# Kernel tuning notes

Hardware: AMD Instinct MI355X
Metric: run time of the kernel (lower is better)

Reference implementation:

```python
import jax, jax.numpy as jnp
import numpy as np

N, E = 10000, 320000
MUL0, MUL1 = 64, 32  # 64x0e + 32x1o
SQ3 = 3.0 ** 0.5
SQ2 = 2.0 ** 0.5


def ssp(v):  # shifted softplus
    return jax.nn.softplus(v) - jnp.log(2.0)


def mlp2(v, W1, W2):  # e3nn FullyConnectedNet style: /sqrt(fan_in), no bias, act between
    h = ssp(v @ (W1 / jnp.sqrt(1.0 * W1.shape[0])))
    return h @ (W2 / jnp.sqrt(1.0 * W2.shape[0]))


def linear_rs(x0, x1, W0, b0, W1):  # per-irrep-type linear with 1/sqrt(fan_in) rescale
    y0 = x0 @ (W0 / jnp.sqrt(1.0 * W0.shape[0])) + b0
    y1 = jnp.einsum('nui,uv->nvi', x1, W1) / jnp.sqrt(1.0 * W1.shape[0])
    return y0, y1


def forward(x, edge_sh, edge_attr, W0p, b0p, W1p, W0n, b0n, W1n, G1, g1b, G2, g2b, F1, F2, L1, L2, WO0, bO0, WO1, WO2, edge_index):
    dst, src = edge_index[0], edge_index[1]
    x0 = x[:, :MUL0]                      # [N,64] scalars
    x1 = x[:, MUL0:].reshape(N, MUL1, 3)  # [N,32,3] l=1 vectors
    # linear_node_pre, then invariant edge features s0 (scalars of dst/src + l1 inner products)
    p0, p1 = linear_rs(x0, x1, W0p, b0p, W1p)
    ip1 = jnp.sum(p1[dst] * p1[src], -1) / SQ3          # [E,32]
    s0 = jnp.concatenate([p0[dst], p0[src], ip1], -1)   # [E,160]
    # NormGate: gate scalars + l1 norms through a 2-layer SiLU MLP
    n1 = jnp.sqrt(jnp.sum(x1 * x1, -1) + 1e-12)         # [N,32]
    f0 = jnp.concatenate([x0, n1], -1)                  # [N,96]
    g = jax.nn.silu(f0 @ G1 + g1b) @ G2 + g2b           # [N,96]
    x0g, x1g = g[:, :MUL0], x1 * g[:, MUL0:, None]
    # linear_node
    x0n, x1n = linear_rs(x0g, x1g, W0n, b0n, W1n)
    # per-edge tensor-product weights: fc_node(edge_attr) * layer_l0(s0)
    w = mlp2(edge_attr, F1, F2) * mlp2(s0, L1, L2)      # [E,224]
    w1, w2, w3, w4, w5 = w[:, :64], w[:, 64:128], w[:, 128:160], w[:, 160:192], w[:, 192:224]
    xs0, xs1 = x0n[src], x1n[src]                       # gather source nodes
    sh0, sh1 = edge_sh[:, 0], edge_sh[:, 1:4]
    # depthwise 'uvu' tensor product paths (w3j constants for l<=1)
    o0a = w1 * xs0 * sh0[:, None]                                        # (0e,0e)->0e  [E,64]
    o0b = w4 * jnp.sum(xs1 * sh1[:, None, :], -1) / SQ3                  # (1o,1o)->0e  [E,32]
    o1a = w2[:, :, None] * xs0[:, :, None] * sh1[:, None, :] / SQ3       # (0e,1o)->1o  [E,64,3]
    o1b = w3[:, :, None] * xs1 * sh0[:, None, None]                      # (1o,0e)->1o  [E,32,3]
    o1c = w5[:, :, None] * jnp.cross(xs1, jnp.broadcast_to(sh1[:, None, :], xs1.shape)) / SQ2  # (1o,1o)->1e [E,32,3]
    ef = jnp.concatenate([o0a, o0b, o1a.reshape(E, -1), o1b.reshape(E, -1), o1c.reshape(E, -1)], -1)  # [E,480]
    out = jax.ops.segment_sum(ef, dst, num_segments=N)  # scatter-add over dst
    # linear_out: 96x0e + 96x1o + 32x1e -> 128x0e + 64x1o + 32x1e
    t0 = out[:, :96]
    t1 = out[:, 96:384].reshape(N, 96, 3)
    t2 = out[:, 384:].reshape(N, 32, 3)
    y0 = t0 @ (WO0 / jnp.sqrt(96.0)) + bO0
    y1 = jnp.einsum('nui,uv->nvi', t1, WO1) / jnp.sqrt(96.0)
    y2 = jnp.einsum('nui,uv->nvi', t2, WO2) / jnp.sqrt(32.0)
    return jnp.concatenate([y0, y1.reshape(N, -1), y2.reshape(N, -1)], -1)  # [N,416]


def setup_inputs():
    key = jax.random.key(0)
    ks = jax.random.split(key, 20)
    rn = lambda k, s: jax.random.normal(k, s, dtype=jnp.float32)
    z = lambda n: jnp.zeros((n,), jnp.float32)
    return dict(
        x=rn(ks[0], (N, 160)),
        edge_sh=rn(ks[1], (E, 4)),
        edge_attr=rn(ks[2], (E, 32)),
        W0p=rn(ks[3], (64, 64)), b0p=z(64), W1p=rn(ks[4], (32, 32)),
        W0n=rn(ks[5], (64, 64)), b0n=z(64), W1n=rn(ks[6], (32, 32)),
        G1=rn(ks[7], (96, 96)) / 96 ** 0.5, g1b=z(96),
        G2=rn(ks[8], (96, 96)) / 96 ** 0.5, g2b=z(96),
        F1=rn(ks[9], (32, 32)), F2=rn(ks[10], (32, 224)),
        L1=rn(ks[11], (160, 32)), L2=rn(ks[12], (32, 224)),
        WO0=rn(ks[13], (96, 128)), bO0=z(128),
        WO1=rn(ks[14], (96, 64)), WO2=rn(ks[15], (32, 32)),
        edge_index=jax.random.randint(ks[16], (2, E), 0, N),
    )


def reference(x, edge_sh, edge_attr, W0p, b0p, W1p, W0n, b0n, W1n, G1, g1b, G2, g2b, F1, F2, L1, L2, WO0, bO0, WO1, WO2, edge_index):
    return forward(x, edge_sh, edge_attr, W0p, b0p, W1p, W0n, b0n, W1n, G1, g1b, G2, g2b, F1, F2, L1, L2, WO0, bO0, WO1, WO2, edge_index)
```

## Files before the change

kernel.cpp:

```cpp
#include <hip/hip_runtime.h>
#include <math.h>

#define NN 10000
#define EE 320000
#define TILE 32

constexpr float INVS32  = 0.17677669529663687f;
constexpr float INVS160 = 0.07905694150420949f;
constexpr float INVS96  = 0.10206207261596575f;
constexpr float INVS3   = 0.5773502691896258f;
constexpr float INVS2   = 0.7071067811865476f;
constexpr float LN2     = 0.6931471805599453f;

typedef short bf16x8 __attribute__((ext_vector_type(8)));
typedef float f32x4  __attribute__((ext_vector_type(4)));

__device__ __forceinline__ float sspf(float v) {
  return fmaxf(v, 0.f) + __logf(1.f + __expf(-fabsf(v))) - LN2;
}
__device__ __forceinline__ ushort f2bf(float f) {
  union { float f; unsigned u; } v; v.f = f;
  unsigned r = v.u + 0x7FFF + ((v.u >> 16) & 1);
  return (ushort)(r >> 16);
}
__device__ __forceinline__ float bf2f(ushort u) {
  return __uint_as_float(((unsigned)u) << 16);
}
__device__ __forceinline__ unsigned pk(float a, float b) {
  return (unsigned)f2bf(a) | ((unsigned)f2bf(b) << 16);
}

__global__ __launch_bounds__(1024) void scan_k(const int* __restrict__ cnt,
                                               int* __restrict__ cursor) {
  __shared__ int s[1024];
  const int t = threadIdx.x;
  int loc[10];
  int sum = 0;
#pragma unroll
  for (int jj = 0; jj < 10; ++jj) {
    int idx = t * 10 + jj;
    int c = (idx < NN) ? cnt[idx] : 0;
    loc[jj] = sum;
    sum += c;
  }
  s[t] = sum;
  __syncthreads();
  for (int d = 1; d < 1024; d <<= 1) {
    int v = (t >= d) ? s[t - d] : 0;
    __syncthreads();
    s[t] += v;
    __syncthreads();
  }
  const int excl = (t > 0) ? s[t - 1] : 0;
#pragma unroll
  for (int jj = 0; jj < 10; ++jj) {
    int idx = t * 10 + jj;
    if (idx < NN) cursor[idx] = excl + loc[jj];
  }
}

__global__ void prep_t_k(const float* __restrict__ F2, const float* __restrict__ L2,
                         const float* __restrict__ WO0, const float* __restrict__ WO1,
                         const float* __restrict__ WO2,
                         const float* __restrict__ F1, const float* __restrict__ L1,
                         const int* __restrict__ ei, int* __restrict__ cnt,
                         ushort* __restrict__ F2Tb, ushort* __restrict__ L2Tb,
                         float* __restrict__ WO0T, float* __restrict__ WO1T,
                         float* __restrict__ WO2T,
                         ushort* __restrict__ F1Tb, ushort* __restrict__ L1cTb) {
  int i = blockIdx.x * 256 + threadIdx.x;
  if (i < EE) atomicAdd(&cnt[ei[i]], 1);
  if (i < 7168) {
    int c = i >> 5, k = i & 31;
    float sc = (c < 64)  ? (1.f / 32.f)
             : (c < 128) ? (INVS3 / 32.f)
             : (c < 160) ? (1.f / 32.f)
             : (c < 192) ? (INVS3 / 32.f)
                         : (INVS2 / 32.f);
    F2Tb[i] = f2bf(F2[k * 224 + c] * sc);
    L2Tb[i] = f2bf(L2[k * 224 + c]);
  } else if (i < 7168 + 12288) {
    int j = i - 7168; int k = j / 96, u = j - k * 96;
    WO0T[j] = WO0[u * 128 + k] * INVS96;
  } else if (i < 7168 + 12288 + 6144) {
    int j = i - 7168 - 12288; int v = j / 96, u = j - v * 96;
    WO1T[j] = WO1[u * 64 + v] * INVS96;
  } else if (i < 7168 + 12288 + 6144 + 1024) {
    int j = i - 7168 - 12288 - 6144; int v = j >> 5, u = j & 31;
    WO2T[j] = WO2[u * 32 + v] * INVS32;
  } else if (i < 26624 + 1024) {
    int j = i - 26624; int n = j >> 5, k = j & 31;
    F1Tb[j] = f2bf(F1[k * 32 + n] * INVS32);
  } else if (i < 27648 + 1024) {
    int j = i - 27648; int n = j >> 5, k = j & 31;
    L1cTb[j] = f2bf(L1[(128 + k) * 32 + n] * INVS160);
  }
}

__global__ __launch_bounds__(64) void node_prep_k(
    const float* __restrict__ x,
    const float* __restrict__ W0p, const float* __restrict__ b0p,
    const float* __restrict__ W1p,
    const float* __restrict__ W0n, const float* __restrict__ b0n,
    const float* __restrict__ W1n,
    const float* __restrict__ G1, const float* __restrict__ g1b,
    const float* __restrict__ G2, const float* __restrict__ g2b,
    const float* __restrict__ L1,
    const int* __restrict__ ei, int* __restrict__ cursor, int* __restrict__ order,
    float* __restrict__ p1w, ushort* __restrict__ x0nb, ushort* __restrict__ x1nb,
    float* __restrict__ Aw, float* __restrict__ Bw)
{
  {
    int gid = blockIdx.x * 64 + threadIdx.x;
#pragma unroll
    for (int r = 0; r < 2; ++r) {
      int e = gid + r * 160000;
      int p = atomicAdd(&cursor[ei[e]], 1);
      order[p] = e;
    }
  }

  const int lane = threadIdx.x;
  const int nb = blockIdx.x * 4;

  __shared__ float sX[4][160];
  __shared__ float sP0[4][64];
  __shared__ float sF0[4][96];
  __shared__ float sH1[4][96];
  __shared__ float sG[4][96];

#pragma unroll
  for (int j = 0; j < 4; ++j) {
    const int n = nb + j;
    sX[j][lane]      = x[n * 160 + lane];
    sX[j][lane + 64] = x[n * 160 + lane + 64];
    if (lane < 32) sX[j][lane + 128] = x[n * 160 + lane + 128];
  }

  {
    float a0 = 0.f, a1 = 0.f, a2 = 0.f, a3 = 0.f;
    for (int i = 0; i < 64; ++i) {
      const float w = W0p[i * 64 + lane];
      a0 = fmaf(sX[0][i], w, a0); a1 = fmaf(sX[1][i], w, a1);
      a2 = fmaf(sX[2][i], w, a2); a3 = fmaf(sX[3][i], w, a3);
    }
    const float b = b0p[lane];
    sP0[0][lane] = a0 * 0.125f + b; sP0[1][lane] = a1 * 0.125f + b;
    sP0[2][lane] = a2 * 0.125f + b; sP0[3][lane] = a3 * 0.125f + b;
#pragma unroll
    for (int j = 0; j < 4; ++j) sF0[j][lane] = sX[j][lane];
  }

  {
    const int o = lane; const int v = o / 3, i_ = o - 3 * v;
    float a0 = 0.f, a1 = 0.f, a2 = 0.f, a3 = 0.f;
    for (int u = 0; u < 32; ++u) {
      const float w = W1p[u * 32 + v];
      a0 = fmaf(sX[0][64 + u * 3 + i_], w, a0);
      a1 = fmaf(sX[1][64 + u * 3 + i_], w, a1);
      a2 = fmaf(sX[2][64 + u * 3 + i_], w, a2);
      a3 = fmaf(sX[3][64 + u * 3 + i_], w, a3);
    }
    p1w[(size_t)(nb + 0) * 96 + o] = a0 * INVS32;
    p1w[(size_t)(nb + 1) * 96 + o] = a1 * INVS32;
    p1w[(size_t)(nb + 2) * 96 + o] = a2 * INVS32;
    p1w[(size_t)(nb + 3) * 96 + o] = a3 * INVS32;
  }
  if (lane < 32) {
    const int o = 64 + lane; const int v = o / 3, i_ = o - 3 * v;
    float a0 = 0.f, a1 = 0.f, a2 = 0.f, a3 = 0.f;
    for (int u = 0; u < 32; ++u) {
      const float w = W1p[u * 32 + v];
      a0 = fmaf(sX[0][64 + u * 3 + i_], w, a0);
      a1 = fmaf(sX[1][64 + u * 3 + i_], w, a1);
      a2 = fmaf(sX[2][64 + u * 3 + i_], w, a2);
      a3 = fmaf(sX[3][64 + u * 3 + i_], w, a3);
    }
    p1w[(size_t)(nb + 0) * 96 + o] = a0 * INVS32;
    p1w[(size_t)(nb + 1) * 96 + o] = a1 * INVS32;
    p1w[(size_t)(nb + 2) * 96 + o] = a2 * INVS32;
    p1w[(size_t)(nb + 3) * 96 + o] = a3 * INVS32;
  }

  if (lane < 32) {
#pragma unroll
    for (int j = 0; j < 4; ++j) {
      float s2 = 1e-12f;
#pragma unroll
      for (int i = 0; i < 3; ++i) { float t = sX[j][64 + lane * 3 + i]; s2 += t * t; }
      sF0[j][64 + lane] = sqrtf(s2);
    }
  }

  {
    const float b = g1b[lane];
    float a0 = b, a1 = b, a2 = b, a3 = b;
    for (int i = 0; i < 96; ++i) {
      const float w = G1[i * 96 + lane];
      a0 = fmaf(sF0[0][i], w, a0); a1 = fmaf(sF0[1][i], w, a1);
      a2 = fmaf(sF0[2][i], w, a2); a3 = fmaf(sF0[3][i], w, a3);
    }
    sH1[0][lane] = a0 / (1.f + __expf(-a0));
    sH1[1][lane] = a1 / (1.f + __expf(-a1));
    sH1[2][lane] = a2 / (1.f + __expf(-a2));
    sH1[3][lane] = a3 / (1.f + __expf(-a3));
  }
  if (lane < 32) {
    const int o = 64 + lane;
    const float b = g1b[o];
    float a0 = b, a1 = b, a2 = b, a3 = b;
    for (int i = 0; i < 96; ++i) {
      const float w = G1[i * 96 + o];
      a0 = fmaf(sF0[0][i], w, a0); a1 = fmaf(sF0[1][i], w, a1);
      a2 = fmaf(sF0[2][i], w, a2); a3 = fmaf(sF0[3][i], w, a3);
    }
    sH1[0][o] = a0 / (1.f + __expf(-a0));
    sH1[1][o] = a1 / (1.f + __expf(-a1));
    sH1[2][o] = a2 / (1.f + __expf(-a2));
    sH1[3][o] = a3 / (1.f + __expf(-a3));
  }

  {
    const float b = g2b[lane];
    float a0 = b, a1 = b, a2 = b, a3 = b;
    for (int i = 0; i < 96; ++i) {
      const float w = G2[i * 96 + lane];
      a0 = fmaf(sH1[0][i], w, a0); a1 = fmaf(sH1[1][i], w, a1);
      a2 = fmaf(sH1[2][i], w, a2); a3 = fmaf(sH1[3][i], w, a3);
    }
    sG[0][lane] = a0; sG[1][lane] = a1; sG[2][lane] = a2; sG[3][lane] = a3;
  }
  if (lane < 32) {
    const int o = 64 + lane;
    const float b = g2b[o];
    float a0 = b, a1 = b, a2 = b, a3 = b;
    for (int i = 0; i < 96; ++i) {
      const float w = G2[i * 96 + o];
      a0 = fmaf(sH1[0][i], w, a0); a1 = fmaf(sH1[1][i], w, a1);
      a2 = fmaf(sH1[2][i], w, a2); a3 = fmaf(sH1[3][i], w, a3);
    }
    sG[0][o] = a0; sG[1][o] = a1; sG[2][o] = a2; sG[3][o] = a3;
  }

  {
    float a0 = 0.f, a1 = 0.f, a2 = 0.f, a3 = 0.f;
    for (int i = 0; i < 64; ++i) {
      const float w = W0n[i * 64 + lane];
      a0 = fmaf(sG[0][i], w, a0); a1 = fmaf(sG[1][i], w, a1);
      a2 = fmaf(sG[2][i], w, a2); a3 = fmaf(sG[3][i], w, a3);
    }
    const float b = b0n[lane];
    x0nb[(size_t)(nb + 0) * 64 + lane] = f2bf(a0 * 0.125f + b);
    x0nb[(size_t)(nb + 1) * 64 + lane] = f2bf(a1 * 0.125f + b);
    x0nb[(size_t)(nb + 2) * 64 + lane] = f2bf(a2 * 0.125f + b);
    x0nb[(size_t)(nb + 3) * 64 + lane] = f2bf(a3 * 0.125f + b);
  }

  {
    const int o = lane; const int v = o / 3, i_ = o - 3 * v;
    float a0 = 0.f, a1 = 0.f, a2 = 0.f, a3 = 0.f;
    for (int u = 0; u < 32; ++u) {
      const float w = W1n[u * 32 + v];
      a0 = fmaf(sX[0][64 + u * 3 + i_] * sG[0][64 + u], w, a0);
      a1 = fmaf(sX[1][64 + u * 3 + i_] * sG[1][64 + u], w, a1);
      a2 = fmaf(sX[2][64 + u * 3 + i_] * sG[2][64 + u], w, a2);
      a3 = fmaf(sX[3][64 + u * 3 + i_] * sG[3][64 + u], w, a3);
    }
    x1nb[(size_t)(nb + 0) * 96 + o] = f2bf(a0 * INVS32);
    x1nb[(size_t)(nb + 1) * 96 + o] = f2bf(a1 * INVS32);
    x1nb[(size_t)(nb + 2) * 96 + o] = f2bf(a2 * INVS32);
    x1nb[(size_t)(nb + 3) * 96 + o] = f2bf(a3 * INVS32);
  }
  if (lane < 32) {
    const int o = 64 + lane; const int v = o / 3, i_ = o - 3 * v;
    float a0 = 0.f, a1 = 0.f, a2 = 0.f, a3 = 0.f;
    for (int u = 0; u < 32; ++u) {
      const float w = W1n[u * 32 + v];
      a0 = fmaf(sX[0][64 + u * 3 + i_] * sG[0][64 + u], w, a0);
      a1 = fmaf(sX[1][64 + u * 3 + i_] * sG[1][64 + u], w, a1);
      a2 = fmaf(sX[2][64 + u * 3 + i_] * sG[2][64 + u], w, a2);
      a3 = fmaf(sX[3][64 + u * 3 + i_] * sG[3][64 + u], w, a3);
    }
    x1nb[(size_t)(nb + 0) * 96 + o] = f2bf(a0 * INVS32);
    x1nb[(size_t)(nb + 1) * 96 + o] = f2bf(a1 * INVS32);
    x1nb[(size_t)(nb + 2) * 96 + o] = f2bf(a2 * INVS32);
    x1nb[(size_t)(nb + 3) * 96 + o] = f2bf(a3 * INVS32);
  }

  if (lane < 32) {
    float a0 = 0.f, a1 = 0.f, a2 = 0.f, a3 = 0.f;
    float c0 = 0.f, c1 = 0.f, c2 = 0.f, c3 = 0.f;
    for (int i = 0; i < 64; ++i) {
      const float wa = L1[i * 32 + lane];
      const float wb = L1[(64 + i) * 32 + lane];
      a0 = fmaf(sP0[0][i], wa, a0); a1 = fmaf(sP0[1][i], wa, a1);
      a2 = fmaf(sP0[2][i], wa, a2); a3 = fmaf(sP0[3][i], wa, a3);
      c0 = fmaf(sP0[0][i], wb, c0); c1 = fmaf(sP0[1][i], wb, c1);
      c2 = fmaf(sP0[2][i], wb, c2); c3 = fmaf(sP0[3][i], wb, c3);
    }
    Aw[(size_t)(nb + 0) * 32 + lane] = a0 * INVS160;
    Aw[(size_t)(nb + 1) * 32 + lane] = a1 * INVS160;
    Aw[(size_t)(nb + 2) * 32 + lane] = a2 * INVS160;
    Aw[(size_t)(nb + 3) * 32 + lane] = a3 * INVS160;
    Bw[(size_t)(nb + 0) * 32 + lane] = c0 * INVS160;
    Bw[(size_t)(nb + 1) * 32 + lane] = c1 * INVS160;
    Bw[(size_t)(nb + 2) * 32 + lane] = c2 * INVS160;
    Bw[(size_t)(nb + 3) * 32 + lane] = c3 * INVS160;
  }
}

__global__ __launch_bounds__(256, 4) void fused_edge_k(
    const float* __restrict__ edge_attr,
    const float* __restrict__ edge_sh,
    const int* __restrict__ ei,
    const ushort* __restrict__ F1Tb, const ushort* __restrict__ L1cTb,
    const ushort* __restrict__ F2Tb, const ushort* __restrict__ L2Tb,
    const float* __restrict__ p1w, const float* __restrict__ Aw,
    const float* __restrict__ Bw,
    const ushort* __restrict__ x0nb, const ushort* __restrict__ x1nb,
    const int* __restrict__ order,
    float* __restrict__ o480p)
{
  const int s0  = blockIdx.x * TILE;
  const int tid = threadIdx.x;

  __shared__ __align__(16) char uMem[32 * 224 * 2];
  ushort (*sW)[224] = (ushort (*)[224])uMem;
  ushort* sEAb = (ushort*)uMem;
  ushort* sIPb = (ushort*)(uMem + 2560);
  float*  sAB  = (float*)(uMem + 5120);

  __shared__ ushort sHF[32][40];
  __shared__ ushort sHL[32][40];
  __shared__ ushort sXS0[32][64];
  __shared__ ushort sXS1[32][96];
  __shared__ __align__(16) float sSH[32][4];
  __shared__ int    sDst[32];

  const int g = tid >> 3, l = tid & 7;
  const int e   = order[s0 + g];
  const int dst = ei[e];
  const int src = ei[EE + e];
  if (l == 0) sDst[g] = dst;

  {
    float4 ea = *(const float4*)(edge_attr + (size_t)e * 32 + l * 4);
    *(unsigned*)&sEAb[g * 40 + l * 4 + 0] = pk(ea.x, ea.y);
    *(unsigned*)&sEAb[g * 40 + l * 4 + 2] = pk(ea.z, ea.w);
  }
  if (l == 1) *(float4*)&sSH[g][0] = *(const float4*)(edge_sh + (size_t)e * 4);
  {
    uint4 v = *(const uint4*)(x0nb + (size_t)src * 64 + l * 8);
    *(uint4*)&sXS0[g][l * 8] = v;
    const uint2* b2 = (const uint2*)(x1nb + (size_t)src * 96 + l * 12);
    uint2 w0 = b2[0], w1 = b2[1], w2 = b2[2];
    *(uint2*)&sXS1[g][l * 12 + 0] = w0;
    *(uint2*)&sXS1[g][l * 12 + 4] = w1;
    *(uint2*)&sXS1[g][l * 12 + 8] = w2;
  }
  {
    const float4* pd = (const float4*)(p1w + (size_t)dst * 96 + l * 12);
    const float4* ps = (const float4*)(p1w + (size_t)src * 96 + l * 12);
    float dp[12], sp[12];
#pragma unroll
    for (int k = 0; k < 3; ++k) {
      float4 v = pd[k]; dp[4*k] = v.x; dp[4*k+1] = v.y; dp[4*k+2] = v.z; dp[4*k+3] = v.w;
      float4 u = ps[k]; sp[4*k] = u.x; sp[4*k+1] = u.y; sp[4*k+2] = u.z; sp[4*k+3] = u.w;
    }
    float ip[4];
#pragma unroll
    for (int vv = 0; vv < 4; ++vv) {
      const int b = 3 * vv;
      ip[vv] = (dp[b] * sp[b] + dp[b+1] * sp[b+1] + dp[b+2] * sp[b+2]) * INVS3;
    }
    *(unsigned*)&sIPb[g * 40 + l * 4 + 0] = pk(ip[0], ip[1]);
    *(unsigned*)&sIPb[g * 40 + l * 4 + 2] = pk(ip[2], ip[3]);
  }
  {
    float4 av = *(const float4*)(Aw + (size_t)dst * 32 + l * 4);
    float4 bv = *(const float4*)(Bw + (size_t)src * 32 + l * 4);
    f32x4 ab;
    ab[0] = av.x + bv.x; ab[1] = av.y + bv.y;
    ab[2] = av.z + bv.z; ab[3] = av.w + bv.w;
    *(f32x4*)&sAB[g * 36 + l * 4] = ab;
  }
  __syncthreads();

  {
    const int wvi  = tid >> 6;
    const int lane = tid & 63;
    const int r = lane & 15;
    const int h = lane >> 4;
    const int qt = wvi & 1;
    const bool isHL = (wvi >= 2);
    const ushort* aBase = isHL ? sIPb : sEAb;
    const ushort* bW    = isHL ? L1cTb : F1Tb;
    ushort* outB = isHL ? &sHL[0][0] : &sHF[0][0];
    bf16x8 afr = *(const bf16x8*)&aBase[(qt * 16 + r) * 40 + h * 8];
#pragma unroll
    for (int ct = 0; ct < 2; ++ct) {
      const int c = ct * 16 + r;
      bf16x8 bfr = *(const bf16x8*)&bW[c * 32 + h * 8];
      f32x4 z = {0.f, 0.f, 0.f, 0.f};
      f32x4 o = __builtin_amdgcn_mfma_f32_16x16x32_bf16(afr, bfr, z, 0, 0, 0);
#pragma unroll
      for (int i = 0; i < 4; ++i) {
        const int q = qt * 16 + h * 4 + i;
        float v = o[i];
        if (isHL) v += sAB[q * 36 + c];
        outB[q * 40 + c] = f2bf(sspf(v));
      }
    }
  }
  __syncthreads();

  {
    const int wv   = tid >> 6;
    const int lane = tid & 63;
    const int r = lane & 15;
    const int h = lane >> 4;
    bf16x8 aF0 = *(const bf16x8*)&sHF[r][h * 8];
    bf16x8 aF1 = *(const bf16x8*)&sHF[16 + r][h * 8];
    bf16x8 aL0 = *(const bf16x8*)&sHL[r][h * 8];
    bf16x8 aL1 = *(const bf16x8*)&sHL[16 + r][h * 8];
    const int ct0 = (wv < 2) ? wv * 4 : 8 + (wv - 2) * 3;
    const int nct = (wv < 2) ? 4 : 3;
    for (int t = 0; t < nct; ++t) {
      const int ct = ct0 + t;
      const int c  = ct * 16 + r;
      bf16x8 bF = *(const bf16x8*)&F2Tb[c * 32 + h * 8];
      bf16x8 bL = *(const bf16x8*)&L2Tb[c * 32 + h * 8];
      f32x4 z = {0.f, 0.f, 0.f, 0.f};
      f32x4 wf0 = __builtin_amdgcn_mfma_f32_16x16x32_bf16(aF0, bF, z, 0, 0, 0);
      f32x4 wl0 = __builtin_amdgcn_mfma_f32_16x16x32_bf16(aL0, bL, z, 0, 0, 0);
      f32x4 wf1 = __builtin_amdgcn_mfma_f32_16x16x32_bf16(aF1, bF, z, 0, 0, 0);
      f32x4 wl1 = __builtin_amdgcn_mfma_f32_16x16x32_bf16(aL1, bL, z, 0, 0, 0);
#pragma unroll
      for (int i = 0; i < 4; ++i) {
        sW[h * 4 + i][c]      = f2bf(wf0[i] * wl0[i]);
        sW[16 + h * 4 + i][c] = f2bf(wf1[i] * wl1[i]);
      }
    }
  }
  __syncthreads();

  if (tid < 128) {
    const int tl = tid;
    float a0 = 0.f, a1 = 0.f, a2 = 0.f, a3 = 0.f;

    for (int q = 0; q < TILE; ++q) {
      const float4 sh = *(const float4*)&sSH[q][0];
      if (tl < 64) {
        const float x0 = bf2f(sXS0[q][tl]);
        const float w0 = bf2f(sW[q][tl]);
        const float w1 = bf2f(sW[q][64 + tl]);
        a0 = fmaf(w0 * x0, sh.x, a0);
        const float t = w1 * x0;
        a1 = fmaf(t, sh.y, a1);
        a2 = fmaf(t, sh.z, a2);
        a3 = fmaf(t, sh.w, a3);
      } else if (tl < 96) {
        const int c = tl - 64;
        const float x0v = bf2f(sXS1[q][3 * c + 0]);
        const float x1v = bf2f(sXS1[q][3 * c + 1]);
        const float x2v = bf2f(sXS1[q][3 * c + 2]);
        const float wb = bf2f(sW[q][160 + c]);
        const float wd = bf2f(sW[q][128 + c]);
        const float d = fmaf(x2v, sh.w, fmaf(x1v, sh.z, x0v * sh.y));
        a0 = fmaf(wb, d, a0);
        const float t = wd * sh.x;
        a1 = fmaf(t, x0v, a1);
        a2 = fmaf(t, x1v, a2);
        a3 = fmaf(t, x2v, a3);
      } else {
        const int u = tl - 96;
        const float x0v = bf2f(sXS1[q][3 * u + 0]);
        const float x1v = bf2f(sXS1[q][3 * u + 1]);
        const float x2v = bf2f(sXS1[q][3 * u + 2]);
        const float wc = bf2f(sW[q][192 + u]);
        a0 = fmaf(wc, fmaf(x1v, sh.w, -(x2v * sh.z)), a0);
        a1 = fmaf(wc, fmaf(x2v, sh.y, -(x0v * sh.w)), a1);
        a2 = fmaf(wc, fmaf(x0v, sh.z, -(x1v * sh.y)), a2);
      }
      const int d = sDst[q];
      const bool fl = (q == TILE - 1) || (sDst[q + 1] != d);
      if (fl) {
        float* dp = o480p + (size_t)d * 480;
        atomicAdd(dp + tl, a0);
        atomicAdd(dp + 128 + tl, a1);
        atomicAdd(dp + 256 + tl, a2);
        if (tl < 96) atomicAdd(dp + 384 + tl, a3);
        a0 = 0.f; a1 = 0.f; a2 = 0.f; a3 = 0.f;
      }
    }
  }
}

__global__ __launch_bounds__(64) void out_wo_k(
    const float* __restrict__ o480p,
    const float* __restrict__ WO0T, const float* __restrict__ WO1T,
    const float* __restrict__ WO2T, const float* __restrict__ bO0,
    float* __restrict__ out)
{
  const int lane = threadIdx.x;
  const int nb = blockIdx.x * 4;
  __shared__ float sO[4][480];
#pragma unroll
  for (int j = 0; j < 4; ++j) {
    const float4* src = (const float4*)(o480p + (size_t)(nb + j) * 480);
    for (int idx = lane; idx < 120; idx += 64)
      *(float4*)&sO[j][idx * 4] = src[idx];
  }

  for (int k = lane; k < 416; k += 64) {
    float y0, y1, y2, y3;
    if (k < 128) {
      const float* wr = WO0T + k * 96;
      float a0 = 0.f, a1 = 0.f, a2 = 0.f, a3 = 0.f;
      for (int u = 0; u < 96; ++u) {
        const float w = wr[u];
        a0 = fmaf(w, sO[0][u], a0); a1 = fmaf(w, sO[1][u], a1);
        a2 = fmaf(w, sO[2][u], a2); a3 = fmaf(w, sO[3][u], a3);
      }
      const float b = bO0[k];
      y0 = a0 + b; y1 = a1 + b; y2 = a2 + b; y3 = a3 + b;
    } else if (k < 320) {
      const int kk = k - 128; const int v = kk / 3; const int i = kk - 3 * v;
      const float* wr = WO1T + v * 96;
      const int base = 128 + 128 * i;
      float a0 = 0.f, a1 = 0.f, a2 = 0.f, a3 = 0.f;
      for (int u = 0; u < 96; ++u) {
        const float w = wr[u];
        a0 = fmaf(w, sO[0][base + u], a0);
        a1 = fmaf(w, sO[1][base + u], a1);
        a2 = fmaf(w, sO[2][base + u], a2);
        a3 = fmaf(w, sO[3][base + u], a3);
      }
      y0 = a0; y1 = a1; y2 = a2; y3 = a3;
    } else {
      const int kk = k - 320; const int v = kk / 3; const int i = kk - 3 * v;
      const float* wr = WO2T + v * 32;
      const int base = 96 + 128 * i;
      float a0 = 0.f, a1 = 0.f, a2 = 0.f, a3 = 0.f;
      for (int u = 0; u < 32; ++u) {
        const float w = wr[u];
        a0 = fmaf(w, sO[0][base + u], a0);
        a1 = fmaf(w, sO[1][base + u], a1);
        a2 = fmaf(w, sO[2][base + u], a2);
        a3 = fmaf(w, sO[3][base + u], a3);
      }
      y0 = a0; y1 = a1; y2 = a2; y3 = a3;
    }
    out[(size_t)(nb + 0) * 416 + k] = y0;
    out[(size_t)(nb + 1) * 416 + k] = y1;
    out[(size_t)(nb + 2) * 416 + k] = y2;
    out[(size_t)(nb + 3) * 416 + k] = y3;
  }
}

extern "C" void kernel_launch(void* const* d_in, const int* in_sizes, int n_in,
                              void* d_out, int out_size, void* d_ws, size_t ws_size,
                              hipStream_t stream) {
  const float* x         = (const float*)d_in[0];
  const float* edge_sh   = (const float*)d_in[1];
  const float* edge_attr = (const float*)d_in[2];
  const float* W0p       = (const float*)d_in[3];
  const float* b0p       = (const float*)d_in[4];
  const float* W1p       = (const float*)d_in[5];
  const float* W0n       = (const float*)d_in[6];
  const float* b0n       = (const float*)d_in[7];
  const float* W1n       = (const float*)d_in[8];
  const float* G1        = (const float*)d_in[9];
  const float* g1b       = (const float*)d_in[10];
  const float* G2        = (const float*)d_in[11];
  const float* g2b       = (const float*)d_in[12];
  const float* F1        = (const float*)d_in[13];
  const float* F2        = (const float*)d_in[14];
  const float* L1        = (const float*)d_in[15];
  const float* L2        = (const float*)d_in[16];
  const float* WO0       = (const float*)d_in[17];
  const float* bO0       = (const float*)d_in[18];
  const float* WO1       = (const float*)d_in[19];
  const float* WO2       = (const float*)d_in[20];
  const int*   ei        = (const int*)d_in[21];
  float* out = (float*)d_out;

  float*  p1w  = (float*)d_ws;
  ushort* x0nb = (ushort*)(p1w + NN * 96);
  ushort* x1nb = x0nb + NN * 64;
  float*  Aw   = (float*)(x1nb + NN * 96);
  float*  Bw   = Aw + NN * 32;
  float*  o480 = Bw + NN * 32;
  int* cnt    = (int*)(o480 + (size_t)NN * 480);
  int* cursor = cnt    + NN;
  int* order  = cursor + NN;
  uintptr_t p = (uintptr_t)(order + EE);
  p = (p + 15) & ~(uintptr_t)15;
  ushort* F2Tb  = (ushort*)p;
  ushort* L2Tb  = F2Tb + 224 * 32;
  ushort* F1Tb  = L2Tb + 224 * 32;
  ushort* L1cTb = F1Tb + 32 * 32;
  uintptr_t p2 = (uintptr_t)(L1cTb + 32 * 32);
  p2 = (p2 + 15) & ~(uintptr_t)15;
  float* WO0T = (float*)p2;
  float* WO1T = WO0T + 128 * 96;
  float* WO2T = WO1T + 64 * 96;

  hipMemsetAsync(cnt, 0, NN * sizeof(int), stream);
  hipMemsetAsync(o480, 0, (size_t)NN * 480 * sizeof(float), stream);
  prep_t_k<<<(EE + 255) / 256, 256, 0, stream>>>(F2, L2, WO0, WO1, WO2, F1, L1,
                                                 ei, cnt,
                                                 F2Tb, L2Tb, WO0T, WO1T, WO2T,
                                                 F1Tb, L1cTb);
  scan_k<<<1, 1024, 0, stream>>>(cnt, cursor);
  node_prep_k<<<NN / 4, 64, 0, stream>>>(x, W0p, b0p, W1p, W0n, b0n, W1n,
                                         G1, g1b, G2, g2b, L1,
                                         ei, cursor, order,
                                         p1w, x0nb, x1nb, Aw, Bw);
  fused_edge_k<<<EE / TILE, 256, 0, stream>>>(edge_attr, edge_sh, ei,
                                              F1Tb, L1cTb, F2Tb, L2Tb,
                                              p1w, Aw, Bw, x0nb, x1nb,
                                              order, o480);
  out_wo_k<<<NN / 4, 64, 0, stream>>>(o480, WO0T, WO1T, WO2T, bO0, out);
}
```

Measured before the change: 285.4 us.

## Store p1 in bf16, transpose edge weights in LDS, pad l1 vectors

The p1 node features are stored as bf16 instead of fp32, which halves the gather traffic for the per-edge inner products. The per-edge weight tile in shared memory is transposed to channel-major with padding, so each thread reads 8 edges' weights in one vector load and MFMA results are written as packed 64-bit stores. The l1 source vectors are repacked into 4-element padded slots so each lane reads one vec3 with a single 64-bit LDS load. The consumer loop is split per thread role, removing per-iteration branching, at the cost of lower p1 precision and more code.

```diff
diff --git a/kernel.cpp b/kernel.cpp
--- a/kernel.cpp
+++ b/kernel.cpp
@@ -25,6 +25,12 @@
 }
 __device__ __forceinline__ float bf2f(ushort u) {
   return __uint_as_float(((unsigned)u) << 16);
+}
+__device__ __forceinline__ float bflo(unsigned w) {
+  return __uint_as_float(w << 16);
+}
+__device__ __forceinline__ float bfhi(unsigned w) {
+  return __uint_as_float(w & 0xFFFF0000u);
 }
 __device__ __forceinline__ unsigned pk(float a, float b) {
   return (unsigned)f2bf(a) | ((unsigned)f2bf(b) << 16);
@@ -107,7 +113,7 @@
     const float* __restrict__ G2, const float* __restrict__ g2b,
     const float* __restrict__ L1,
     const int* __restrict__ ei, int* __restrict__ cursor, int* __restrict__ order,
-    float* __restrict__ p1w, ushort* __restrict__ x0nb, ushort* __restrict__ x1nb,
+    ushort* __restrict__ p1b, ushort* __restrict__ x0nb, ushort* __restrict__ x1nb,
     float* __restrict__ Aw, float* __restrict__ Bw)
 {
   {
@@ -161,10 +167,10 @@
       a2 = fmaf(sX[2][64 + u * 3 + i_], w, a2);
       a3 = fmaf(sX[3][64 + u * 3 + i_], w, a3);
     }
-    p1w[(size_t)(nb + 0) * 96 + o] = a0 * INVS32;
-    p1w[(size_t)(nb + 1) * 96 + o] = a1 * INVS32;
-    p1w[(size_t)(nb + 2) * 96 + o] = a2 * INVS32;
-    p1w[(size_t)(nb + 3) * 96 + o] = a3 * INVS32;
+    p1b[(size_t)(nb + 0) * 96 + o] = f2bf(a0 * INVS32);
+    p1b[(size_t)(nb + 1) * 96 + o] = f2bf(a1 * INVS32);
+    p1b[(size_t)(nb + 2) * 96 + o] = f2bf(a2 * INVS32);
+    p1b[(size_t)(nb + 3) * 96 + o] = f2bf(a3 * INVS32);
   }
   if (lane < 32) {
     const int o = 64 + lane; const int v = o / 3, i_ = o - 3 * v;
@@ -176,10 +182,10 @@
       a2 = fmaf(sX[2][64 + u * 3 + i_], w, a2);
       a3 = fmaf(sX[3][64 + u * 3 + i_], w, a3);
     }
-    p1w[(size_t)(nb + 0) * 96 + o] = a0 * INVS32;
-    p1w[(size_t)(nb + 1) * 96 + o] = a1 * INVS32;
-    p1w[(size_t)(nb + 2) * 96 + o] = a2 * INVS32;
-    p1w[(size_t)(nb + 3) * 96 + o] = a3 * INVS32;
+    p1b[(size_t)(nb + 0) * 96 + o] = f2bf(a0 * INVS32);
+    p1b[(size_t)(nb + 1) * 96 + o] = f2bf(a1 * INVS32);
+    p1b[(size_t)(nb + 2) * 96 + o] = f2bf(a2 * INVS32);
+    p1b[(size_t)(nb + 3) * 96 + o] = f2bf(a3 * INVS32);
   }
 
   if (lane < 32) {
@@ -315,7 +321,7 @@
     const int* __restrict__ ei,
     const ushort* __restrict__ F1Tb, const ushort* __restrict__ L1cTb,
     const ushort* __restrict__ F2Tb, const ushort* __restrict__ L2Tb,
-    const float* __restrict__ p1w, const float* __restrict__ Aw,
+    const ushort* __restrict__ p1b, const float* __restrict__ Aw,
     const float* __restrict__ Bw,
     const ushort* __restrict__ x0nb, const ushort* __restrict__ x1nb,
     const int* __restrict__ order,
@@ -324,8 +330,8 @@
   const int s0  = blockIdx.x * TILE;
   const int tid = threadIdx.x;
 
-  __shared__ __align__(16) char uMem[32 * 224 * 2];
-  ushort (*sW)[224] = (ushort (*)[224])uMem;
+  __shared__ __align__(16) char uMem[224 * 40 * 2];
+  ushort* sWT  = (ushort*)uMem;
   ushort* sEAb = (ushort*)uMem;
   ushort* sIPb = (ushort*)(uMem + 2560);
   float*  sAB  = (float*)(uMem + 5120);
@@ -333,7 +339,7 @@
   __shared__ ushort sHF[32][40];
   __shared__ ushort sHL[32][40];
   __shared__ ushort sXS0[32][64];
-  __shared__ ushort sXS1[32][96];
+  __shared__ ushort sXS1p[32 * 136];
   __shared__ __align__(16) float sSH[32][4];
   __shared__ int    sDst[32];
 
@@ -353,28 +359,34 @@
     uint4 v = *(const uint4*)(x0nb + (size_t)src * 64 + l * 8);
     *(uint4*)&sXS0[g][l * 8] = v;
     const uint2* b2 = (const uint2*)(x1nb + (size_t)src * 96 + l * 12);
-    uint2 w0 = b2[0], w1 = b2[1], w2 = b2[2];
-    *(uint2*)&sXS1[g][l * 12 + 0] = w0;
-    *(uint2*)&sXS1[g][l * 12 + 4] = w1;
-    *(uint2*)&sXS1[g][l * 12 + 8] = w2;
-  }
-  {
-    const float4* pd = (const float4*)(p1w + (size_t)dst * 96 + l * 12);
-    const float4* ps = (const float4*)(p1w + (size_t)src * 96 + l * 12);
-    float dp[12], sp[12];
-#pragma unroll
-    for (int k = 0; k < 3; ++k) {
-      float4 v = pd[k]; dp[4*k] = v.x; dp[4*k+1] = v.y; dp[4*k+2] = v.z; dp[4*k+3] = v.w;
-      float4 u = ps[k]; sp[4*k] = u.x; sp[4*k+1] = u.y; sp[4*k+2] = u.z; sp[4*k+3] = u.w;
-    }
-    float ip[4];
-#pragma unroll
-    for (int vv = 0; vv < 4; ++vv) {
-      const int b = 3 * vv;
-      ip[vv] = (dp[b] * sp[b] + dp[b+1] * sp[b+1] + dp[b+2] * sp[b+2]) * INVS3;
-    }
-    *(unsigned*)&sIPb[g * 40 + l * 4 + 0] = pk(ip[0], ip[1]);
-    *(unsigned*)&sIPb[g * 40 + l * 4 + 2] = pk(ip[2], ip[3]);
+    uint2 b0 = b2[0], b1 = b2[1], b2v = b2[2];
+    uint2 t0; t0.x = b0.x;                               t0.y = b0.y;
+    uint2 t1; t1.x = (b0.y >> 16) | (b1.x << 16);        t1.y = b1.x >> 16;
+    uint2 t2; t2.x = b1.y;                               t2.y = b2v.x;
+    uint2 t3; t3.x = (b2v.x >> 16) | (b2v.y << 16);      t3.y = b2v.y >> 16;
+    ushort* base = &sXS1p[g * 136 + l * 16];
+    *(uint2*)&base[0]  = t0;
+    *(uint2*)&base[4]  = t1;
+    *(uint2*)&base[8]  = t2;
+    *(uint2*)&base[12] = t3;
+  }
+  {
+    const uint2* pd2 = (const uint2*)(p1b + (size_t)dst * 96 + l * 12);
+    const uint2* ps2 = (const uint2*)(p1b + (size_t)src * 96 + l * 12);
+    uint2 d0 = pd2[0], d1 = pd2[1], d2 = pd2[2];
+    uint2 s0v = ps2[0], s1v = ps2[1], s2v = ps2[2];
+    const float dp0 = bflo(d0.x),  dp1 = bfhi(d0.x),  dp2 = bflo(d0.y),  dp3 = bfhi(d0.y);
+    const float dp4 = bflo(d1.x),  dp5 = bfhi(d1.x),  dp6 = bflo(d1.y),  dp7 = bfhi(d1.y);
+    const float dp8 = bflo(d2.x),  dp9 = bfhi(d2.x),  dp10 = bflo(d2.y), dp11 = bfhi(d2.y);
+    const float sp0 = bflo(s0v.x), sp1 = bfhi(s0v.x), sp2 = bflo(s0v.y), sp3 = bfhi(s0v.y);
+    const float sp4 = bflo(s1v.x), sp5 = bfhi(s1v.x), sp6 = bflo(s1v.y), sp7 = bfhi(s1v.y);
+    const float sp8 = bflo(s2v.x), sp9 = bfhi(s2v.x), sp10 = bflo(s2v.y), sp11 = bfhi(s2v.y);
+    const float ip0 = (dp0*sp0 + dp1*sp1 + dp2*sp2) * INVS3;
+    const float ip1 = (dp3*sp3 + dp4*sp4 + dp5*sp5) * INVS3;
+    const float ip2 = (dp6*sp6 + dp7*sp7 + dp8*sp8) * INVS3;
+    const float ip3 = (dp9*sp9 + dp10*sp10 + dp11*sp11) * INVS3;
+    *(unsigned*)&sIPb[g * 40 + l * 4 + 0] = pk(ip0, ip1);
+    *(unsigned*)&sIPb[g * 40 + l * 4 + 2] = pk(ip2, ip3);
   }
   {
     float4 av = *(const float4*)(Aw + (size_t)dst * 32 + l * 4);
@@ -435,11 +447,12 @@
       f32x4 wl0 = __builtin_amdgcn_mfma_f32_16x16x32_bf16(aL0, bL, z, 0, 0, 0);
       f32x4 wf1 = __builtin_amdgcn_mfma_f32_16x16x32_bf16(aF1, bF, z, 0, 0, 0);
       f32x4 wl1 = __builtin_amdgcn_mfma_f32_16x16x32_bf16(aL1, bL, z, 0, 0, 0);
-#pragma unroll
-      for (int i = 0; i < 4; ++i) {
-        sW[h * 4 + i][c]      = f2bf(wf0[i] * wl0[i]);
-        sW[16 + h * 4 + i][c] = f2bf(wf1[i] * wl1[i]);
-      }
+      uint2 lo; lo.x = pk(wf0[0]*wl0[0], wf0[1]*wl0[1]);
+                lo.y = pk(wf0[2]*wl0[2], wf0[3]*wl0[3]);
+      uint2 hi; hi.x = pk(wf1[0]*wl1[0], wf1[1]*wl1[1]);
+                hi.y = pk(wf1[2]*wl1[2], wf1[3]*wl1[3]);
+      *(uint2*)&sWT[c * 40 + h * 4]      = lo;
+      *(uint2*)&sWT[c * 40 + 16 + h * 4] = hi;
     }
   }
   __syncthreads();
@@ -448,49 +461,93 @@
     const int tl = tid;
     float a0 = 0.f, a1 = 0.f, a2 = 0.f, a3 = 0.f;
 
-    for (int q = 0; q < TILE; ++q) {
-      const float4 sh = *(const float4*)&sSH[q][0];
-      if (tl < 64) {
-        const float x0 = bf2f(sXS0[q][tl]);
-        const float w0 = bf2f(sW[q][tl]);
-        const float w1 = bf2f(sW[q][64 + tl]);
-        a0 = fmaf(w0 * x0, sh.x, a0);
-        const float t = w1 * x0;
-        a1 = fmaf(t, sh.y, a1);
-        a2 = fmaf(t, sh.z, a2);
-        a3 = fmaf(t, sh.w, a3);
-      } else if (tl < 96) {
-        const int c = tl - 64;
-        const float x0v = bf2f(sXS1[q][3 * c + 0]);
-        const float x1v = bf2f(sXS1[q][3 * c + 1]);
-        const float x2v = bf2f(sXS1[q][3 * c + 2]);
-        const float wb = bf2f(sW[q][160 + c]);
-        const float wd = bf2f(sW[q][128 + c]);
-        const float d = fmaf(x2v, sh.w, fmaf(x1v, sh.z, x0v * sh.y));
-        a0 = fmaf(wb, d, a0);
-        const float t = wd * sh.x;
-        a1 = fmaf(t, x0v, a1);
-        a2 = fmaf(t, x1v, a2);
-        a3 = fmaf(t, x2v, a3);
-      } else {
-        const int u = tl - 96;
-        const float x0v = bf2f(sXS1[q][3 * u + 0]);
-        const float x1v = bf2f(sXS1[q][3 * u + 1]);
-        const float x2v = bf2f(sXS1[q][3 * u + 2]);
-        const float wc = bf2f(sW[q][192 + u]);
-        a0 = fmaf(wc, fmaf(x1v, sh.w, -(x2v * sh.z)), a0);
-        a1 = fmaf(wc, fmaf(x2v, sh.y, -(x0v * sh.w)), a1);
-        a2 = fmaf(wc, fmaf(x0v, sh.z, -(x1v * sh.y)), a2);
+    if (tl < 64) {
+      for (int p4 = 0; p4 < 4; ++p4) {
+        const int q0 = p4 * 8;
+        bf16x8 w0v = *(const bf16x8*)&sWT[tl * 40 + q0];
+        bf16x8 w1v = *(const bf16x8*)&sWT[(64 + tl) * 40 + q0];
+#pragma unroll
+        for (int j = 0; j < 8; ++j) {
+          const int q = q0 + j;
+          const float4 sh = *(const float4*)&sSH[q][0];
+          const float x0 = bf2f(sXS0[q][tl]);
+          const float w0 = bf2f((ushort)w0v[j]);
+          const float w1 = bf2f((ushort)w1v[j]);
+          a0 = fmaf(w0 * x0, sh.x, a0);
+          const float t = w1 * x0;
+          a1 = fmaf(t, sh.y, a1);
+          a2 = fmaf(t, sh.z, a2);
+          a3 = fmaf(t, sh.w, a3);
+          const int d = sDst[q];
+          if ((q == TILE - 1) || (sDst[q + 1] != d)) {
+            float* dp = o480p + (size_t)d * 480;
+            atomicAdd(dp + tl, a0);
+            atomicAdd(dp + 128 + tl, a1);
+            atomicAdd(dp + 256 + tl, a2);
+            atomicAdd(dp + 384 + tl, a3);
+            a0 = 0.f; a1 = 0.f; a2 = 0.f; a3 = 0.f;
+          }
+        }
       }
-      const int d = sDst[q];
-      const bool fl = (q == TILE - 1) || (sDst[q + 1] != d);
-      if (fl) {
-        float* dp = o480p + (size_t)d * 480;
-        atomicAdd(dp + tl, a0);
-        atomicAdd(dp + 128 + tl, a1);
-        atomicAdd(dp + 256 + tl, a2);
-        if (tl < 96) atomicAdd(dp + 384 + tl, a3);
-        a0 = 0.f; a1 = 0.f; a2 = 0.f; a3 = 0.f;
+    } else if (tl < 96) {
+      const int c = tl - 64;
+      for (int p4 = 0; p4 < 4; ++p4) {
+        const int q0 = p4 * 8;
+        bf16x8 wbv = *(const bf16x8*)&sWT[(160 + c) * 40 + q0];
+        bf16x8 wdv = *(const bf16x8*)&sWT[(128 + c) * 40 + q0];
+#pragma unroll
+        for (int j = 0; j < 8; ++j) {
+          const int q = q0 + j;
+          const float4 sh = *(const float4*)&sSH[q][0];
+          uint2 t3 = *(const uint2*)&sXS1p[q * 136 + c * 4];
+          const float x0v = bflo(t3.x);
+          const float x1v = bfhi(t3.x);
+          const float x2v = bflo(t3.y);
+          const float wb = bf2f((ushort)wbv[j]);
+          const float wd = bf2f((ushort)wdv[j]);
+          const float d2 = fmaf(x2v, sh.w, fmaf(x1v, sh.z, x0v * sh.y));
+          a0 = fmaf(wb, d2, a0);
+          const float t = wd * sh.x;
+          a1 = fmaf(t, x0v, a1);
+          a2 = fmaf(t, x1v, a2);
+          a3 = fmaf(t, x2v, a3);
+          const int d = sDst[q];
+          if ((q == TILE - 1) || (sDst[q + 1] != d)) {
+            float* dp = o480p + (size_t)d * 480;
+            atomicAdd(dp + tl, a0);
+            atomicAdd(dp + 128 + tl, a1);
+            atomicAdd(dp + 256 + tl, a2);
+            atomicAdd(dp + 384 + tl, a3);
+            a0 = 0.f; a1 = 0.f; a2 = 0.f; a3 = 0.f;
+          }
+        }
+      }
+    } else {
+      const int u = tl - 96;
+      for (int p4 = 0; p4 < 4; ++p4) {
+        const int q0 = p4 * 8;
+        bf16x8 wcv = *(const bf16x8*)&sWT[(192 + u) * 40 + q0];
+#pragma unroll
+        for (int j = 0; j < 8; ++j) {
+          const int q = q0 + j;
+          const float4 sh = *(const float4*)&sSH[q][0];
+          uint2 t3 = *(const uint2*)&sXS1p[q * 136 + u * 4];
+          const float x0v = bflo(t3.x);
+          const float x1v = bfhi(t3.x);
+          const float x2v = bflo(t3.y);
+          const float wc = bf2f((ushort)wcv[j]);
+          a0 = fmaf(wc, fmaf(x1v, sh.w, -(x2v * sh.z)), a0);
+          a1 = fmaf(wc, fmaf(x2v, sh.y, -(x0v * sh.w)), a1);
+          a2 = fmaf(wc, fmaf(x0v, sh.z, -(x1v * sh.y)), a2);
+          const int d = sDst[q];
+          if ((q == TILE - 1) || (sDst[q + 1] != d)) {
+            float* dp = o480p + (size_t)d * 480;
+            atomicAdd(dp + tl, a0);
+            atomicAdd(dp + 128 + tl, a1);
+            atomicAdd(dp + 256 + tl, a2);
+            a0 = 0.f; a1 = 0.f; a2 = 0.f;
+          }
+        }
       }
     }
   }
@@ -585,8 +642,8 @@
   const int*   ei        = (const int*)d_in[21];
   float* out = (float*)d_out;
 
-  float*  p1w  = (float*)d_ws;
-  ushort* x0nb = (ushort*)(p1w + NN * 96);
+  ushort* p1b  = (ushort*)d_ws;
+  ushort* x0nb = p1b + NN * 96;
   ushort* x1nb = x0nb + NN * 64;
   float*  Aw   = (float*)(x1nb + NN * 96);
   float*  Bw   = Aw + NN * 32;
@@ -616,10 +673,10 @@
   node_prep_k<<<NN / 4, 64, 0, stream>>>(x, W0p, b0p, W1p, W0n, b0n, W1n,
                                          G1, g1b, G2, g2b, L1,
                                          ei, cursor, order,
-                                         p1w, x0nb, x1nb, Aw, Bw);
+                                         p1b, x0nb, x1nb, Aw, Bw);
   fused_edge_k<<<EE / TILE, 256, 0, stream>>>(edge_attr, edge_sh, ei,
                                               F1Tb, L1cTb, F2Tb, L2Tb,
-                                              p1w, Aw, Bw, x0nb, x1nb,
+                                              p1b, Aw, Bw, x0nb, x1nb,
                                               order, o480);
   out_wo_k<<<NN / 4, 64, 0, stream>>>(o480, WO0T, WO1T, WO2T, bO0, out);
 }
```

Result: faster. 259.9 us (median of 3 runs) (-8.9%).
